# Kernel tuning notes

Measured on AMD Instinct MI355X. Metric: run time of the kernel, lower is better.

The kernel has to match this reference:

```python
import jax, jax.numpy as jnp
import numpy as np


def _rotate_half(x):
    half = x.shape[-1] // 2
    x1, x2 = x[..., :half], x[..., half:]
    return jnp.concatenate([-x2, x1], axis=-1)


def setup_inputs() -> dict:
    key = jax.random.key(0)
    ks = jax.random.split(key, 7)
    B, T, D, H, Hd = 4, 2048, 1024, 16, 64
    x = jax.random.normal(ks[0], (B, T, D), dtype=jnp.float32)
    # RoPE tables (realistic: built from inv freqs)
    inv_freq = 1.0 / (10000.0 ** (jnp.arange(0, Hd, 2, dtype=jnp.float32) / Hd))
    pos = jnp.arange(T, dtype=jnp.float32)
    freqs = pos[:, None] * inv_freq[None, :]            # (T, Hd/2)
    emb = jnp.concatenate([freqs, freqs], axis=-1)       # (T, Hd)
    cos, sin = jnp.cos(emb), jnp.sin(emb)
    s = 1.0 / np.sqrt(D)
    w_q = jax.random.normal(ks[1], (D, D), dtype=jnp.float32) * s
    w_k = jax.random.normal(ks[2], (D, D), dtype=jnp.float32) * s
    w_v = jax.random.normal(ks[3], (D, D), dtype=jnp.float32) * s
    w_o = jax.random.normal(ks[4], (D, D), dtype=jnp.float32) * s
    return {"x": x, "cos": cos, "sin": sin, "w_q": w_q, "w_k": w_k, "w_v": w_v, "w_o": w_o}


def reference(x, cos, sin, w_q, w_k, w_v, w_o):
    B, T, D = x.shape
    H = 16
    Hd = D // H
    scale = Hd ** -0.5
    # nn.Linear(bias=False): y = x @ W.T
    q = (x @ w_q.T).reshape(B, T, H, Hd).transpose(0, 2, 1, 3)  # (B,H,T,Hd)
    k = (x @ w_k.T).reshape(B, T, H, Hd).transpose(0, 2, 1, 3)
    v = (x @ w_v.T).reshape(B, T, H, Hd).transpose(0, 2, 1, 3)
    c = cos[None, None, :, :]
    s = sin[None, None, :, :]
    q = q * c + _rotate_half(q) * s
    k = k * c + _rotate_half(k) * s
    scores = jnp.einsum('bhqd,bhkd->bhqk', q, k) * scale  # (B,H,T,T)
    causal = jnp.tril(jnp.ones((T, T), dtype=bool))
    scores = jnp.where(causal[None, None], scores, -jnp.inf)
    weights = jax.nn.softmax(scores, axis=-1)
    out = jnp.einsum('bhqk,bhkd->bhqd', weights, v)
    out = out.transpose(0, 2, 1, 3).reshape(B, T, D)
    return out @ w_o.T
```

## Files before the change

kernel.cpp:

```cpp
#include <hip/hip_runtime.h>
#include <stdint.h>

typedef __attribute__((ext_vector_type(8))) __bf16 bf16x8;
typedef __attribute__((ext_vector_type(4))) float floatx4;


__device__ __forceinline__ unsigned short f2bf(float f) {
    unsigned int u = __float_as_uint(f);
    u += 0x7FFFu + ((u >> 16) & 1u);
    return (unsigned short)(u >> 16);
}
__device__ __forceinline__ unsigned int pack2bf(float lo, float hi) {
    return (unsigned int)f2bf(lo) | ((unsigned int)f2bf(hi) << 16);
}
__device__ __forceinline__ unsigned int packtrunc(float lo, float hi) {
    return __builtin_amdgcn_perm(__float_as_uint(hi), __float_as_uint(lo), 0x07060302u);
}

__device__ __forceinline__ void gl_lds16(const void* g, void* l) {
    __builtin_amdgcn_global_load_lds(
        (const __attribute__((address_space(1))) void*)g,
        (__attribute__((address_space(3))) void*)l, 16, 0, 0);
}


__global__ void cvt_all(const float* __restrict__ x,  const float* __restrict__ wq,
                        const float* __restrict__ wk, const float* __restrict__ wv,
                        const float* __restrict__ wo,
                        unsigned short* __restrict__ xb,  unsigned short* __restrict__ wqb,
                        unsigned short* __restrict__ wkb, unsigned short* __restrict__ wvb,
                        unsigned short* __restrict__ wob) {
    int i = blockIdx.x * blockDim.x + threadIdx.x;
    const float* in; unsigned short* out; int idx;
    if (i < 2097152) { in = x; out = xb; idx = i; }
    else {
        int j = i - 2097152; int wsel = j >> 18; idx = j & 262143;
        in  = (wsel == 0) ? wq  : (wsel == 1) ? wk  : (wsel == 2) ? wv  : wo;
        out = (wsel == 0) ? wqb : (wsel == 1) ? wkb : (wsel == 2) ? wvb : wob;
    }
    float4 v = ((const float4*)in)[idx];
    ushort4 o;
    o.x = f2bf(v.x); o.y = f2bf(v.y); o.z = f2bf(v.z); o.w = f2bf(v.w);
    ((ushort4*)out)[idx] = o;
}


template<int MODE>
__global__ __launch_bounds__(256, 2)
void gemm_bt(const unsigned short* __restrict__ A,
             const unsigned short* __restrict__ Wq,
             const unsigned short* __restrict__ Wk,
             const float* __restrict__ cosp,
             const float* __restrict__ sinp,
             unsigned short* __restrict__ outq,
             unsigned short* __restrict__ outk,
             unsigned short* __restrict__ outvt,
             float* __restrict__ outf)
{
    constexpr int K = 1024;
    __shared__ __align__(16) unsigned short As[128 * 32];
    __shared__ __align__(16) unsigned short Bs[128 * 32];

    const int t    = threadIdx.x;
    const int w    = t >> 6;
    const int lane = t & 63;
    const int c    = lane & 15;
    const int quad = lane >> 4;
    const int wr   = w >> 1, wc = w & 1;

    const int m0 = blockIdx.x * 128;
    int which, n0;
    const unsigned short* W;
    if constexpr (MODE == 0) {
        which = blockIdx.y >> 3;
        n0    = (blockIdx.y & 7) * 128;
        W     = which ? Wk : Wq;
    } else {
        which = 0;
        n0    = blockIdx.y * 128;
        W     = Wq;
    }

    const int srow = t >> 2;
    const int scol = (t & 3) * 8;
    const unsigned short* ga0 = A + (size_t)(m0 + srow) * K + scol;
    const unsigned short* ga1 = A + (size_t)(m0 + srow + 64) * K + scol;
    const unsigned short* gb0 = W + (size_t)(n0 + srow) * K + scol;
    const unsigned short* gb1 = W + (size_t)(n0 + srow + 64) * K + scol;
    void* lA0 = (char*)As + t * 16;
    void* lA1 = (char*)As + 4096 + t * 16;
    void* lB0 = (char*)Bs + t * 16;
    void* lB1 = (char*)Bs + 4096 + t * 16;

    floatx4 acc[4][4] = {};

    const int arow = wr * 64;
    const int brow = wc * 64;

    for (int k0 = 0; k0 < K; k0 += 32) {
        __syncthreads();
        gl_lds16(ga0 + k0, lA0);
        gl_lds16(ga1 + k0, lA1);
        gl_lds16(gb0 + k0, lB0);
        gl_lds16(gb1 + k0, lB1);
        __syncthreads();
        bf16x8 af[4], bfr[4];
        #pragma unroll
        for (int mi = 0; mi < 4; mi++)
            af[mi] = *(const bf16x8*)&As[(arow + mi * 16 + c) * 32 + quad * 8];
        #pragma unroll
        for (int ni = 0; ni < 4; ni++)
            bfr[ni] = *(const bf16x8*)&Bs[(brow + ni * 16 + c) * 32 + quad * 8];
        if constexpr (MODE == 2) {
            #pragma unroll
            for (int mi = 0; mi < 4; mi++)
                #pragma unroll
                for (int ni = 0; ni < 4; ni++)
                    acc[mi][ni] = __builtin_amdgcn_mfma_f32_16x16x32_bf16(
                        af[mi], bfr[ni], acc[mi][ni], 0, 0, 0);
        } else {
            #pragma unroll
            for (int mi = 0; mi < 4; mi++)
                #pragma unroll
                for (int ni = 0; ni < 4; ni++)
                    acc[mi][ni] = __builtin_amdgcn_mfma_f32_16x16x32_bf16(
                        bfr[ni], af[mi], acc[mi][ni], 0, 0, 0);
        }
    }

    if constexpr (MODE == 1) {
        #pragma unroll
        for (int mi = 0; mi < 4; mi++) {
            int m = m0 + wr * 64 + mi * 16 + c;
            #pragma unroll
            for (int ni = 0; ni < 4; ni++) {
                int n = n0 + wc * 64 + ni * 16 + quad * 4;
                *(floatx4*)&outf[(size_t)m * 1024 + n] = acc[mi][ni];
            }
        }
    } else if constexpr (MODE == 2) {
        const int hh = (n0 + wc * 64) >> 6;
        #pragma unroll
        for (int mi = 0; mi < 4; mi++) {
            int t0 = m0 + wr * 64 + mi * 16 + quad * 4;
            int b = t0 >> 11, tt0 = t0 & 2047;
            #pragma unroll
            for (int ni = 0; ni < 4; ni++) {
                int d = ni * 16 + c;
                uint2 pk;
                pk.x = pack2bf(acc[mi][ni][0], acc[mi][ni][1]);
                pk.y = pack2bf(acc[mi][ni][2], acc[mi][ni][3]);
                *(uint2*)&outvt[((size_t)((b * 16 + hh) * 64 + d)) * 2048 + tt0] = pk;
            }
        }
    } else {
        const int hh = (n0 + wc * 64) >> 6;
        unsigned short* dst = which ? outk : outq;
        const float scale = which ? 1.0f : (0.125f * 1.44269504088896f);
        #pragma unroll
        for (int mi = 0; mi < 4; mi++) {
            int m = m0 + wr * 64 + mi * 16 + c;
            int b = m >> 11, tt = m & 2047;
            size_t obase = ((size_t)(b * 16 + hh) * 2048 + tt) * 64;
            #pragma unroll
            for (int ni = 0; ni < 4; ni++) {
                int d0 = ni * 16 + quad * 4;
                float4 cv = *(const float4*)&cosp[tt * 64 + d0];
                float4 sv = *(const float4*)&sinp[tt * 64 + d0];
                float ca[4] = {cv.x, cv.y, cv.z, cv.w};
                float sa[4] = {sv.x, sv.y, sv.z, sv.w};
                float vq[4];
                #pragma unroll
                for (int r = 0; r < 4; r++) {
                    float pr  = acc[mi][ni ^ 2][r];
                    float rot = (ni & 2) ? pr : -pr;
                    vq[r] = (acc[mi][ni][r] * ca[r] + rot * sa[r]) * scale;
                }
                uint2 pk;
                pk.x = pack2bf(vq[0], vq[1]);
                pk.y = pack2bf(vq[2], vq[3]);
                *(uint2*)&dst[obase + d0] = pk;
            }
        }
    }
}

__global__ __launch_bounds__(256)
void flash_attn(const unsigned short* __restrict__ Q,
                const unsigned short* __restrict__ Kg,
                const unsigned short* __restrict__ Vt,
                unsigned short* __restrict__ O)
{
    __shared__ __align__(16) unsigned short Ks[2][64 * 64];
    __shared__ __align__(16) unsigned short Vs[2][64 * 64];

    const int t    = threadIdx.x;
    const int w    = t >> 6;
    const int lane = t & 63;
    const int c    = lane & 15;
    const int quad = lane >> 4;

    const int bh = blockIdx.x;
    const int b  = bh >> 4, h = bh & 15;

    const unsigned short* qp = Q  + (size_t)bh * 2048 * 64;
    const unsigned short* kp = Kg + (size_t)bh * 2048 * 64;
    const unsigned short* vp = Vt + (size_t)bh * 64 * 2048;

    const int srow = t >> 3;
    const int sj   = (t & 7) ^ (srow & 7);

    const int qi = 31 - (int)blockIdx.y;
    const int q0 = qi * 64;
    const int qb = q0 + w * 16;

    bf16x8 qf[2];
    #pragma unroll
    for (int dc = 0; dc < 2; dc++)
        qf[dc] = *(const bf16x8*)&qp[(size_t)(qb + c) * 64 + dc * 32 + quad * 8];

    union { unsigned short us[8]; bf16x8 v; } one8;
    #pragma unroll
    for (int j = 0; j < 8; j++) one8.us[j] = 0x3F80;

    floatx4 o[4] = {};
    floatx4 lacc = {};

    #pragma unroll
    for (int ch = 0; ch < 2; ch++) {
        int kr = ch * 32 + srow;
        gl_lds16(kp + (size_t)kr * 64 + sj * 8, (char*)&Ks[0][0] + ch * 4096 + t * 16);
        gl_lds16(vp + (size_t)kr * 2048 + sj * 8, (char*)&Vs[0][0] + ch * 4096 + t * 16);
    }

    const int iters = qi + 1;
    for (int it = 0; it < iters; it++) {
        const int cur = it & 1;
        const int kt0 = it * 64;
        __syncthreads();
        if (it + 1 < iters) {
            const int kt1 = kt0 + 64;
            #pragma unroll
            for (int ch = 0; ch < 2; ch++) {
                int kr = ch * 32 + srow;
                gl_lds16(kp + (size_t)(kt1 + kr) * 64 + sj * 8,
                         (char*)&Ks[cur ^ 1][0] + ch * 4096 + t * 16);
                gl_lds16(vp + (size_t)kr * 2048 + kt1 + sj * 8,
                         (char*)&Vs[cur ^ 1][0] + ch * 4096 + t * 16);
            }
        }
        const unsigned short* KsC = &Ks[cur][0];
        const unsigned short* VsC = &Vs[cur][0];

        floatx4 s[4] = {};
        #pragma unroll
        for (int dc = 0; dc < 2; dc++) {
            const int phys = (dc * 4 + quad) ^ (c & 7);
            #pragma unroll
            for (int mt = 0; mt < 4; mt++) {
                bf16x8 kb = *(const bf16x8*)&KsC[(mt * 16 + c) * 64 + phys * 8];
                s[mt] = __builtin_amdgcn_mfma_f32_16x16x32_bf16(kb, qf[dc], s[mt], 0, 0, 0);
            }
        }

        if (it == iters - 1) {
            #pragma unroll
            for (int mt = 0; mt < 4; mt++) {
                int keyb = kt0 + mt * 16 + quad * 4;
                #pragma unroll
                for (int r = 0; r < 4; r++)
                    if (keyb + r > qb + c) s[mt][r] = -1e30f;
            }
        }

        uint2 pk[4];
        #pragma unroll
        for (int mt = 0; mt < 4; mt++) {
            float p0 = __builtin_amdgcn_exp2f(s[mt][0]);
            float p1 = __builtin_amdgcn_exp2f(s[mt][1]);
            float p2 = __builtin_amdgcn_exp2f(s[mt][2]);
            float p3 = __builtin_amdgcn_exp2f(s[mt][3]);
            pk[mt].x = packtrunc(p0, p1);
            pk[mt].y = packtrunc(p2, p3);
        }

        #pragma unroll
        for (int kc = 0; kc < 2; kc++) {
            unsigned int x0 = pk[2 * kc].x;
            unsigned int x1 = pk[2 * kc].y;
            unsigned int x2 = pk[2 * kc + 1].x;
            unsigned int x3 = pk[2 * kc + 1].y;
            asm("v_permlane32_swap_b32 %0, %1" : "+v"(x0), "+v"(x2));
            asm("v_permlane32_swap_b32 %0, %1" : "+v"(x1), "+v"(x3));
            asm("v_permlane16_swap_b32 %0, %1" : "+v"(x0), "+v"(x2));
            asm("v_permlane16_swap_b32 %0, %1" : "+v"(x1), "+v"(x3));
            union { unsigned int u[4]; bf16x8 v; } ap;
            ap.u[0] = x0; ap.u[1] = x1; ap.u[2] = x2; ap.u[3] = x3;

            lacc = __builtin_amdgcn_mfma_f32_16x16x32_bf16(ap.v, one8.v, lacc, 0, 0, 0);

            const int phys = (kc * 4 + quad) ^ (c & 7);
            #pragma unroll
            for (int ni = 0; ni < 4; ni++) {
                bf16x8 vb = *(const bf16x8*)&VsC[(ni * 16 + c) * 64 + phys * 8];
                o[ni] = __builtin_amdgcn_mfma_f32_16x16x32_bf16(ap.v, vb, o[ni], 0, 0, 0);
            }
        }
    }

    #pragma unroll
    for (int r = 0; r < 4; r++) {
        float linv = __builtin_amdgcn_rcpf(lacc[r]);
        int qrow = qb + quad * 4 + r;
        size_t base = ((size_t)(b * 2048 + qrow)) * 1024 + h * 64;
        #pragma unroll
        for (int ni = 0; ni < 4; ni++)
            O[base + ni * 16 + c] = f2bf(o[ni][r] * linv);
    }
}


extern "C" void kernel_launch(void* const* d_in, const int* in_sizes, int n_in,
                              void* d_out, int out_size, void* d_ws, size_t ws_size,
                              hipStream_t stream) {
    const float* x    = (const float*)d_in[0];
    const float* cosp = (const float*)d_in[1];
    const float* sinp = (const float*)d_in[2];
    const float* wq   = (const float*)d_in[3];
    const float* wk   = (const float*)d_in[4];
    const float* wv   = (const float*)d_in[5];
    const float* wo   = (const float*)d_in[6];

    char* ws = (char*)d_ws;
    const size_t MB = 1024 * 1024;
    unsigned short* xb   = (unsigned short*)(ws + 0);
    unsigned short* attn = (unsigned short*)(ws + 0);
    unsigned short* wqb  = (unsigned short*)(ws + 16 * MB);
    unsigned short* wkb  = (unsigned short*)(ws + 18 * MB);
    unsigned short* wvb  = (unsigned short*)(ws + 20 * MB);
    unsigned short* wob  = (unsigned short*)(ws + 22 * MB);
    unsigned short* qbuf = (unsigned short*)(ws + 24 * MB);
    unsigned short* kbuf = (unsigned short*)(ws + 40 * MB);
    unsigned short* vtb  = (unsigned short*)(ws + 56 * MB);

    cvt_all<<<dim3(12288), 256, 0, stream>>>(x, wq, wk, wv, wo,
                                             xb, wqb, wkb, wvb, wob);

    gemm_bt<0><<<dim3(64, 16), 256, 0, stream>>>(xb, wqb, wkb, cosp, sinp,
                                                 qbuf, kbuf, nullptr, nullptr);
    gemm_bt<2><<<dim3(64, 8), 256, 0, stream>>>(xb, wvb, nullptr, nullptr, nullptr,
                                                nullptr, nullptr, vtb, nullptr);

    flash_attn<<<dim3(64, 32), 256, 0, stream>>>(qbuf, kbuf, vtb, attn);

    gemm_bt<1><<<dim3(64, 8), 256, 0, stream>>>(attn, wob, nullptr, nullptr, nullptr,
                                                nullptr, nullptr, nullptr, (float*)d_out);
}
```

Before: 255.0 us.

## Double-buffer GEMM LDS tiles to overlap global loads with MFMA

The shared A and B tiles in the projection GEMM become ping-pong buffers. The next K-slice is issued into the other buffer with direct global-to-LDS loads while the MFMAs run on the current slice, which removes one barrier per iteration. The goal is to hide global memory latency behind the matrix math. The cost is twice the LDS per block, and the overlap may be lost if the compiler inserts a conservative vmcnt wait before the LDS reads.

```diff
diff --git a/kernel.cpp b/kernel.cpp
--- a/kernel.cpp
+++ b/kernel.cpp
@@ -57,9 +57,10 @@
              unsigned short* __restrict__ outvt,
              float* __restrict__ outf)
 {
-    constexpr int K = 1024;
-    __shared__ __align__(16) unsigned short As[128 * 32];
-    __shared__ __align__(16) unsigned short Bs[128 * 32];
+    constexpr int K  = 1024;
+    constexpr int NT = K / 32;
+    __shared__ __align__(16) unsigned short As[2][128 * 32];
+    __shared__ __align__(16) unsigned short Bs[2][128 * 32];
 
     const int t    = threadIdx.x;
     const int w    = t >> 6;
@@ -87,30 +88,34 @@
     const unsigned short* ga1 = A + (size_t)(m0 + srow + 64) * K + scol;
     const unsigned short* gb0 = W + (size_t)(n0 + srow) * K + scol;
     const unsigned short* gb1 = W + (size_t)(n0 + srow + 64) * K + scol;
-    void* lA0 = (char*)As + t * 16;
-    void* lA1 = (char*)As + 4096 + t * 16;
-    void* lB0 = (char*)Bs + t * 16;
-    void* lB1 = (char*)Bs + 4096 + t * 16;
 
     floatx4 acc[4][4] = {};
 
     const int arow = wr * 64;
     const int brow = wc * 64;
 
-    for (int k0 = 0; k0 < K; k0 += 32) {
+    auto stage = [&](int buf, int k0) {
+        char* la = (char*)&As[buf][0] + t * 16;
+        char* lb = (char*)&Bs[buf][0] + t * 16;
+        gl_lds16(ga0 + k0, la);
+        gl_lds16(ga1 + k0, la + 4096);
+        gl_lds16(gb0 + k0, lb);
+        gl_lds16(gb1 + k0, lb + 4096);
+    };
+
+    stage(0, 0);
+
+    for (int it = 0; it < NT; ++it) {
+        const int cur = it & 1;
         __syncthreads();
-        gl_lds16(ga0 + k0, lA0);
-        gl_lds16(ga1 + k0, lA1);
-        gl_lds16(gb0 + k0, lB0);
-        gl_lds16(gb1 + k0, lB1);
-        __syncthreads();
+        if (it + 1 < NT) stage(cur ^ 1, (it + 1) * 32);
         bf16x8 af[4], bfr[4];
         #pragma unroll
         for (int mi = 0; mi < 4; mi++)
-            af[mi] = *(const bf16x8*)&As[(arow + mi * 16 + c) * 32 + quad * 8];
+            af[mi] = *(const bf16x8*)&As[cur][(arow + mi * 16 + c) * 32 + quad * 8];
         #pragma unroll
         for (int ni = 0; ni < 4; ni++)
-            bfr[ni] = *(const bf16x8*)&Bs[(brow + ni * 16 + c) * 32 + quad * 8];
+            bfr[ni] = *(const bf16x8*)&Bs[cur][(brow + ni * 16 + c) * 32 + quad * 8];
         if constexpr (MODE == 2) {
             #pragma unroll
             for (int mi = 0; mi < 4; mi++)
```

After: 259.9 us. Within noise of the previous version (+2.0%).

## Merge QKV GEMMs into one launch with K=64 swizzled LDS tiles

Applied to the files above, without the earlier changes.

Folds the V projection into the Q/K projection kernel, so a single launch with 24 column tile groups writes Q, K and transposed V, and one kernel launch is removed. The GEMM k-step doubles from 32 to 64, halving the barrier and load rounds per output tile. An XOR swizzle is applied to the LDS tile layout to avoid bank conflicts on fragment reads. LDS per block doubles, which may reduce occupancy, and a runtime branch on the mode now sits inside the MFMA loop.

```diff
diff --git a/kernel.cpp b/kernel.cpp
--- a/kernel.cpp
+++ b/kernel.cpp
@@ -50,6 +50,7 @@
 void gemm_bt(const unsigned short* __restrict__ A,
              const unsigned short* __restrict__ Wq,
              const unsigned short* __restrict__ Wk,
+             const unsigned short* __restrict__ Wv,
              const float* __restrict__ cosp,
              const float* __restrict__ sinp,
              unsigned short* __restrict__ outq,
@@ -58,8 +59,8 @@
              float* __restrict__ outf)
 {
     constexpr int K = 1024;
-    __shared__ __align__(16) unsigned short As[128 * 32];
-    __shared__ __align__(16) unsigned short Bs[128 * 32];
+    __shared__ __align__(16) unsigned short As[128 * 64];
+    __shared__ __align__(16) unsigned short Bs[128 * 64];
 
     const int t    = threadIdx.x;
     const int w    = t >> 6;
@@ -69,62 +70,67 @@
     const int wr   = w >> 1, wc = w & 1;
 
     const int m0 = blockIdx.x * 128;
-    int which, n0;
+    int which3, n0;
     const unsigned short* W;
     if constexpr (MODE == 0) {
-        which = blockIdx.y >> 3;
-        n0    = (blockIdx.y & 7) * 128;
-        W     = which ? Wk : Wq;
+        which3 = blockIdx.y >> 3;
+        n0     = (blockIdx.y & 7) * 128;
+        W      = (which3 == 0) ? Wq : (which3 == 1) ? Wk : Wv;
     } else {
-        which = 0;
-        n0    = blockIdx.y * 128;
-        W     = Wq;
-    }
-
-    const int srow = t >> 2;
-    const int scol = (t & 3) * 8;
-    const unsigned short* ga0 = A + (size_t)(m0 + srow) * K + scol;
-    const unsigned short* ga1 = A + (size_t)(m0 + srow + 64) * K + scol;
-    const unsigned short* gb0 = W + (size_t)(n0 + srow) * K + scol;
-    const unsigned short* gb1 = W + (size_t)(n0 + srow + 64) * K + scol;
-    void* lA0 = (char*)As + t * 16;
-    void* lA1 = (char*)As + 4096 + t * 16;
-    void* lB0 = (char*)Bs + t * 16;
-    void* lB1 = (char*)Bs + 4096 + t * 16;
+        which3 = 0;
+        n0     = blockIdx.y * 128;
+        W      = Wq;
+    }
+    const bool vmode = (MODE == 0) && (which3 == 2);
+
+    const int srow = t >> 3;
+    const int sj   = ((t & 7) ^ (srow & 7)) * 8;
+    const unsigned short* ga[4];
+    const unsigned short* gb[4];
+    #pragma unroll
+    for (int j = 0; j < 4; j++) {
+        ga[j] = A + (size_t)(m0 + srow + 32 * j) * K + sj;
+        gb[j] = W + (size_t)(n0 + srow + 32 * j) * K + sj;
+    }
 
     floatx4 acc[4][4] = {};
 
     const int arow = wr * 64;
     const int brow = wc * 64;
 
-    for (int k0 = 0; k0 < K; k0 += 32) {
+    for (int k0 = 0; k0 < K; k0 += 64) {
         __syncthreads();
-        gl_lds16(ga0 + k0, lA0);
-        gl_lds16(ga1 + k0, lA1);
-        gl_lds16(gb0 + k0, lB0);
-        gl_lds16(gb1 + k0, lB1);
+        #pragma unroll
+        for (int j = 0; j < 4; j++) {
+            gl_lds16(ga[j] + k0, (char*)As + j * 4096 + t * 16);
+            gl_lds16(gb[j] + k0, (char*)Bs + j * 4096 + t * 16);
+        }
         __syncthreads();
-        bf16x8 af[4], bfr[4];
-        #pragma unroll
-        for (int mi = 0; mi < 4; mi++)
-            af[mi] = *(const bf16x8*)&As[(arow + mi * 16 + c) * 32 + quad * 8];
-        #pragma unroll
-        for (int ni = 0; ni < 4; ni++)
-            bfr[ni] = *(const bf16x8*)&Bs[(brow + ni * 16 + c) * 32 + quad * 8];
-        if constexpr (MODE == 2) {
+        #pragma unroll
+        for (int kk = 0; kk < 2; kk++) {
+            const int phys = (((kk << 2) | quad) ^ (c & 7)) * 8;
+            bf16x8 af[4], bfr[4];
             #pragma unroll
             for (int mi = 0; mi < 4; mi++)
+                af[mi] = *(const bf16x8*)&As[(arow + mi * 16 + c) * 64 + phys];
+            #pragma unroll
+            for (int ni = 0; ni < 4; ni++)
+                bfr[ni] = *(const bf16x8*)&Bs[(brow + ni * 16 + c) * 64 + phys];
+            if (vmode) {
                 #pragma unroll
-                for (int ni = 0; ni < 4; ni++)
-                    acc[mi][ni] = __builtin_amdgcn_mfma_f32_16x16x32_bf16(
-                        af[mi], bfr[ni], acc[mi][ni], 0, 0, 0);
-        } else {
-            #pragma unroll
-            for (int mi = 0; mi < 4; mi++)
+                for (int mi = 0; mi < 4; mi++)
+                    #pragma unroll
+                    for (int ni = 0; ni < 4; ni++)
+                        acc[mi][ni] = __builtin_amdgcn_mfma_f32_16x16x32_bf16(
+                            af[mi], bfr[ni], acc[mi][ni], 0, 0, 0);
+            } else {
                 #pragma unroll
-                for (int ni = 0; ni < 4; ni++)
-                    acc[mi][ni] = __builtin_amdgcn_mfma_f32_16x16x32_bf16(
-                        bfr[ni], af[mi], acc[mi][ni], 0, 0, 0);
+                for (int mi = 0; mi < 4; mi++)
+                    #pragma unroll
+                    for (int ni = 0; ni < 4; ni++)
+                        acc[mi][ni] = __builtin_amdgcn_mfma_f32_16x16x32_bf16(
+                            bfr[ni], af[mi], acc[mi][ni], 0, 0, 0);
+            }
         }
     }
 
@@ -138,7 +144,7 @@
                 *(floatx4*)&outf[(size_t)m * 1024 + n] = acc[mi][ni];
             }
         }
-    } else if constexpr (MODE == 2) {
+    } else if (vmode) {
         const int hh = (n0 + wc * 64) >> 6;
         #pragma unroll
         for (int mi = 0; mi < 4; mi++) {
@@ -155,8 +161,8 @@
         }
     } else {
         const int hh = (n0 + wc * 64) >> 6;
-        unsigned short* dst = which ? outk : outq;
-        const float scale = which ? 1.0f : (0.125f * 1.44269504088896f);
+        unsigned short* dst = which3 ? outk : outq;
+        const float scale = which3 ? 1.0f : (0.125f * 1.44269504088896f);
         #pragma unroll
         for (int mi = 0; mi < 4; mi++) {
             int m = m0 + wr * 64 + mi * 16 + c;
@@ -346,13 +352,11 @@
     cvt_all<<<dim3(12288), 256, 0, stream>>>(x, wq, wk, wv, wo,
                                              xb, wqb, wkb, wvb, wob);
 
-    gemm_bt<0><<<dim3(64, 16), 256, 0, stream>>>(xb, wqb, wkb, cosp, sinp,
-                                                 qbuf, kbuf, nullptr, nullptr);
-    gemm_bt<2><<<dim3(64, 8), 256, 0, stream>>>(xb, wvb, nullptr, nullptr, nullptr,
-                                                nullptr, nullptr, vtb, nullptr);
+    gemm_bt<0><<<dim3(64, 24), 256, 0, stream>>>(xb, wqb, wkb, wvb, cosp, sinp,
+                                                 qbuf, kbuf, vtb, nullptr);
 
     flash_attn<<<dim3(64, 32), 256, 0, stream>>>(qbuf, kbuf, vtb, attn);
 
-    gemm_bt<1><<<dim3(64, 8), 256, 0, stream>>>(attn, wob, nullptr, nullptr, nullptr,
+    gemm_bt<1><<<dim3(64, 8), 256, 0, stream>>>(attn, wob, nullptr, nullptr, nullptr, nullptr,
                                                 nullptr, nullptr, nullptr, (float*)d_out);
 }
```

Result: faster. 243.8 us, median of 3 (-4.4%).
